# Performance work log

Hardware: AMD Instinct MI355X
Metric: run time of the kernel (lower is better)

## Reference

```python
import jax, jax.numpy as jnp
import numpy as np

D_MODEL = 1024
NUM_HEADS = 16
D_K = D_MODEL // NUM_HEADS
HEADS_DIST = [4, 4, 2, 2, 4]  # [token, statement, data_flow, control_flow, standard]
HYP_DF = 5.0
HYP_CF = 5.0
NEG_INF = -1000000000.0
B, S = 4, 1024


def _head_group_weights():
    # one-hot-per-group weight vectors of length NUM_HEADS
    ws = []
    start = 0
    for n in HEADS_DIST:
        w = np.zeros(NUM_HEADS, dtype=np.float32)
        w[start:start + n] = 1.0
        ws.append(jnp.asarray(w))
        start += n
    return ws  # tok_w, stmt_w, df_w, cf_w, std_w


def setup_inputs() -> dict:
    key = jax.random.key(0)
    ks = jax.random.split(key, 12)
    f32 = jnp.float32
    inp = {
        'Q': jax.random.normal(ks[0], (B, S, D_MODEL), f32),
        'K': jax.random.normal(ks[1], (B, S, D_MODEL), f32),
        'V': jax.random.normal(ks[2], (B, S, D_MODEL), f32),
        'token': jax.random.randint(ks[3], (B, S, S), 0, 2).astype(f32),
        'statement': jax.random.randint(ks[4], (B, S, S), 0, 2).astype(f32),
        'data_flow': jax.random.randint(ks[5], (B, S, S), 0, 2).astype(f32),
        'control_flow': jax.random.randint(ks[6], (B, S, S), 0, 2).astype(f32),
        'zero_matrix': jnp.zeros((B, S, S), f32),
        'mask': jax.random.randint(ks[7], (B, 1, S, S), 0, 2).astype(jnp.int32),
        # linear layer params (torch nn.Linear: y = x @ W.T + b)
        'Wq': jax.random.normal(ks[8], (D_MODEL, D_MODEL), f32) * 0.02,
        'bq': jnp.zeros((D_MODEL,), f32),
        'Wk': jax.random.normal(ks[9], (D_MODEL, D_MODEL), f32) * 0.02,
        'bk': jnp.zeros((D_MODEL,), f32),
        'Wv': jax.random.normal(ks[10], (D_MODEL, D_MODEL), f32) * 0.02,
        'bv': jnp.zeros((D_MODEL,), f32),
        'Wo': jax.random.normal(ks[11], (D_MODEL, D_MODEL), f32) * 0.02,
        'bo': jnp.zeros((D_MODEL,), f32),
    }
    return inp


def _split_heads(x):
    b, s, _ = x.shape
    return x.reshape(b, s, NUM_HEADS, D_K).transpose(0, 2, 1, 3)  # (B,H,S,dk)


def reference(Q, K, V, token, statement, data_flow, control_flow, zero_matrix,
              mask, Wq, bq, Wk, bk, Wv, bv, Wo, bo):
    tok_w, stmt_w, df_w, cf_w, _ = _head_group_weights()

    Qh = _split_heads(Q @ Wq.T + bq)
    Kh = _split_heads(K @ Wk.T + bk)
    Vh = _split_heads(V @ Wv.T + bv)

    scores = jnp.einsum('bhqd,bhkd->bhqk', Qh, Kh) / jnp.sqrt(jnp.float32(D_K))

    # local mask: -1e9 * token for token-heads, -1e9 * statement for statement-heads,
    # zero_matrix (zeros) elsewhere — expressed via per-head group weights instead of
    # the original redundant stack.
    w = lambda v: v[None, :, None, None]  # (1,H,1,1)
    local_mask = NEG_INF * (w(tok_w) * token[:, None] + w(stmt_w) * statement[:, None])
    # global enhance: |scores * (hyp_df*data_flow | hyp_cf*control_flow)| on their heads
    enhance_adj = (HYP_DF * w(df_w) * data_flow[:, None]
                   + HYP_CF * w(cf_w) * control_flow[:, None])
    global_enhance = jnp.abs(enhance_adj * scores)

    scores = scores + local_mask + global_enhance
    scores = jnp.where(mask == 0, NEG_INF, scores)

    probs = jax.nn.softmax(scores, axis=-1)  # (B,H,S,S)
    ctx = jnp.einsum('bhqk,bhkd->bhqd', probs, Vh)
    out = ctx.transpose(0, 2, 1, 3).reshape(B, S, D_MODEL)
    return out @ Wo.T + bo
```

## Files before the change

### kernel.cpp

```cpp
#include <hip/hip_runtime.h>
#include <stdint.h>

typedef unsigned short u16;
typedef unsigned int   u32;
typedef unsigned char  u8;
typedef __attribute__((ext_vector_type(4))) float f32x4;
typedef __attribute__((ext_vector_type(8))) __bf16 bf16x8;
typedef __attribute__((ext_vector_type(2))) unsigned int u32x2;
typedef __attribute__((ext_vector_type(4))) unsigned int u32x4;

#define MFMA16(a, b, c) __builtin_amdgcn_mfma_f32_16x16x32_bf16((a), (b), (c), 0, 0, 0)

__device__ __forceinline__ u16 f2bf(float f) {
  u32 u = __float_as_uint(f);
  return (u16)((u + 0x7fffu + ((u >> 16) & 1u)) >> 16);
}

__device__ __forceinline__ void gl_lds16(const void* g, void* l) {
  __builtin_amdgcn_global_load_lds((const __attribute__((address_space(1))) u32*)g,
                                   (__attribute__((address_space(3))) u32*)l, 16, 0, 0);
}

__device__ __forceinline__ u32 cvtpk(float a, float b) {
  u32 r;
  asm("v_cvt_pk_bf16_f32 %0, %1, %2" : "=v"(r) : "v"(a), "v"(b));
  return r;
}

__device__ __forceinline__ float exp2_hw(float x) {
  float r;
  asm("v_exp_f32 %0, %1" : "=v"(r) : "v"(x));
  return r;
}

__device__ __forceinline__ void plswap32(u32& x, u32& y) {
  u32x2 r = __builtin_amdgcn_permlane32_swap(x, y, false, false);
  x = r.x; y = r.y;
}
__device__ __forceinline__ void plswap16(u32& x, u32& y) {
  u32x2 r = __builtin_amdgcn_permlane16_swap(x, y, false, false);
  x = r.x; y = r.y;
}

__device__ __forceinline__ float redsum_lg(float v) {
  u32 x = __float_as_uint(v), y = x;
  plswap16(x, y);
  float m = __uint_as_float(x) + __uint_as_float(y);
  u32 a = __float_as_uint(m), b = a;
  plswap32(a, b);
  return __uint_as_float(a) + __uint_as_float(b);
}

__device__ __forceinline__ u32 pbit(float t, float s, float d, float c, int m) {
  const u32 nm = (m == 0) ? 1u : 0u;
  u32 r = (t != 0.0f ? 1u : 0u) | (s != 0.0f ? 2u : 0u) | (d != 0.0f ? 4u : 0u) |
          (c != 0.0f ? 8u : 0u) | ((1u - nm) << 4);
  r |= (((t != 0.0f ? 1u : 0u) | nm) << 5) | (((s != 0.0f ? 1u : 0u) | nm) << 6) | (nm << 7);
  return r;
}

__global__ void __launch_bounds__(256) pack_kernel(const float4* __restrict__ tok, const float4* __restrict__ st,
                                                   const float4* __restrict__ df, const float4* __restrict__ cf,
                                                   const int4* __restrict__ msk, u32* __restrict__ pko) {
  const int i = blockIdx.x * 256 + threadIdx.x;
  const int b = i >> 18, rem = i & 262143, q = rem >> 8, k4 = rem & 255;
  const int t = k4 >> 4, nk = (k4 >> 2) & 3, lg = k4 & 3;
  const u32 widx = ((u32)(b * 64 + (q >> 4)) * 16 + t) * 256 + (q & 15) * 16 + lg * 4 + nk;
  float4 vt = tok[i], vs = st[i], vd = df[i], vc = cf[i];
  int4 vm = msk[i];
  u32 b0 = pbit(vt.x, vs.x, vd.x, vc.x, vm.x);
  u32 b1 = pbit(vt.y, vs.y, vd.y, vc.y, vm.y);
  u32 b2 = pbit(vt.z, vs.z, vd.z, vc.z, vm.z);
  u32 b3 = pbit(vt.w, vs.w, vd.w, vc.w, vm.w);
  pko[widx] = b0 | (b1 << 8) | (b2 << 16) | (b3 << 24);
}

__global__ void __launch_bounds__(256) cvt_kernel(const float4* __restrict__ Q, const float4* __restrict__ K,
                                                  const float4* __restrict__ V, const float4* __restrict__ Wq,
                                                  const float4* __restrict__ Wk, const float4* __restrict__ Wv,
                                                  const float4* __restrict__ Wo, ushort4* __restrict__ oQ,
                                                  ushort4* __restrict__ oK, ushort4* __restrict__ oV,
                                                  ushort4* __restrict__ oWq, ushort4* __restrict__ oWk,
                                                  ushort4* __restrict__ oWv, ushort4* __restrict__ oWo) {
  const int bid = blockIdx.x;
  const float4* src;
  ushort4* dst;
  int base;
  if (bid < 1024)      { src = Q;  dst = oQ;  base = bid; }
  else if (bid < 2048) { src = K;  dst = oK;  base = bid - 1024; }
  else if (bid < 3072) { src = V;  dst = oV;  base = bid - 2048; }
  else if (bid < 3328) { src = Wq; dst = oWq; base = bid - 3072; }
  else if (bid < 3584) { src = Wk; dst = oWk; base = bid - 3328; }
  else if (bid < 3840) { src = Wv; dst = oWv; base = bid - 3584; }
  else                 { src = Wo; dst = oWo; base = bid - 3840; }
  const int i0 = base * 1024 + threadIdx.x;
#pragma unroll
  for (int u = 0; u < 4; u++) {
    const int i = i0 + u * 256;
    float4 v = src[i];
    dst[i] = make_ushort4(f2bf(v.x), f2bf(v.y), f2bf(v.z), f2bf(v.w));
  }
}

__global__ void __launch_bounds__(256) gemm_qkv(const u16* __restrict__ Abase, const u16* __restrict__ Wbase,
                                                const float* __restrict__ bq, const float* __restrict__ bk,
                                                const float* __restrict__ bv, u16* __restrict__ Obase) {
  __shared__ u16 smA[2][4096];
  __shared__ u16 smB[2][4096];
  const int fb = blockIdx.x;
  const int lid = (fb & 7) * 96 + (fb >> 3);
  const int z = lid >> 8;
  const int m0 = ((lid & 255) >> 3) * 128;
  const int n0 = (lid & 7) * 128;
  const u16* A = Abase + (size_t)z * 4194304;
  const u16* W = Wbase + (size_t)z * 1048576;
  const float* bias = (z == 0) ? bq : (z == 1) ? bk : bv;
  u16* Out = Obase + (size_t)z * 4194304;
  const int t = threadIdx.x;
  const int w = t >> 6, l = t & 63;
  const int l15 = l & 15, lg = l >> 4;
  const int wr = w >> 1, wc = w & 1;
  f32x4 acc[4][4] = {};
  const int srow = w * 16 + (l >> 2);
  const int scol_src = (((l & 3) ^ ((l >> 2) & 3))) * 8;
  const int scol_dst = (l & 3) * 8;
  const u16* Ab = A + (size_t)(m0 + srow) * 1024 + scol_src;
  const u16* Wb = W + (size_t)(n0 + srow) * 1024 + scol_src;
  const int soff = srow * 32 + scol_dst;
  const int c0g = (lg ^ (l15 & 3)) * 8;

  gl_lds16(Ab, &smA[0][soff]);
  gl_lds16(Ab + (size_t)64 * 1024, &smA[0][soff + 64 * 32]);
  gl_lds16(Wb, &smB[0][soff]);
  gl_lds16(Wb + (size_t)64 * 1024, &smB[0][soff + 64 * 32]);

  for (int it = 0; it < 32; it++) {
    __syncthreads();
    if (it < 31) {
      const int kk = (it + 1) * 32;
      const int nb = (it + 1) & 1;
      gl_lds16(Ab + kk, &smA[nb][soff]);
      gl_lds16(Ab + kk + (size_t)64 * 1024, &smA[nb][soff + 64 * 32]);
      gl_lds16(Wb + kk, &smB[nb][soff]);
      gl_lds16(Wb + kk + (size_t)64 * 1024, &smB[nb][soff + 64 * 32]);
    }
    const u16* bA = smA[it & 1];
    const u16* bB = smB[it & 1];
    bf16x8 af[4], bv_[4];
#pragma unroll
    for (int i = 0; i < 4; i++) af[i] = *(const bf16x8*)(bA + (wr * 64 + i * 16 + l15) * 32 + c0g);
#pragma unroll
    for (int i = 0; i < 4; i++) bv_[i] = *(const bf16x8*)(bB + (wc * 64 + i * 16 + l15) * 32 + c0g);
#pragma unroll
    for (int i = 0; i < 4; i++)
#pragma unroll
      for (int j = 0; j < 4; j++) acc[i][j] = MFMA16(af[i], bv_[j], acc[i][j]);
  }
#pragma unroll
  for (int j = 0; j < 4; j++) {
    const int n = n0 + wc * 64 + j * 16 + l15;
    const float bvj = bias[n];
#pragma unroll
    for (int i = 0; i < 4; i++) {
      const int mbase = m0 + wr * 64 + i * 16 + lg * 4;
      if (z < 2) {
#pragma unroll
        for (int r = 0; r < 4; r++) {
          const int m = mbase + r;
          Out[((size_t)((m >> 10) * 16 + (n >> 6)) << 16) + (size_t)(m & 1023) * 64 + (n & 63)] =
              f2bf(acc[i][j][r] + bvj);
        }
      } else {
        size_t off = ((size_t)((mbase >> 10) * 16 + (n >> 6)) << 16) + (size_t)(n & 63) * 1024 + (mbase & 1023);
        *(ushort4*)(Out + off) = make_ushort4(f2bf(acc[i][j][0] + bvj), f2bf(acc[i][j][1] + bvj),
                                              f2bf(acc[i][j][2] + bvj), f2bf(acc[i][j][3] + bvj));
      }
    }
  }
}

__global__ void __launch_bounds__(256) gemm_out(const u16* __restrict__ A, const u16* __restrict__ W,
                                                const float* __restrict__ bias, float* __restrict__ Out) {
  __shared__ u16 smA[2][4096];
  __shared__ u16 smB[2][4096];
  const int fb = blockIdx.x;
  const int lid = (fb & 7) * 32 + (fb >> 3);
  const int m0 = (lid >> 3) * 128;
  const int n0 = (lid & 7) * 128;
  const int t = threadIdx.x;
  const int w = t >> 6, l = t & 63;
  const int l15 = l & 15, lg = l >> 4;
  const int wr = w >> 1, wc = w & 1;
  f32x4 acc[4][4] = {};
  const int srow = w * 16 + (l >> 2);
  const int scol_src = (((l & 3) ^ ((l >> 2) & 3))) * 8;
  const int scol_dst = (l & 3) * 8;
  const u16* Ab = A + (size_t)(m0 + srow) * 1024 + scol_src;
  const u16* Wb = W + (size_t)(n0 + srow) * 1024 + scol_src;
  const int soff = srow * 32 + scol_dst;
  const int c0g = (lg ^ (l15 & 3)) * 8;

  gl_lds16(Ab, &smA[0][soff]);
  gl_lds16(Ab + (size_t)64 * 1024, &smA[0][soff + 64 * 32]);
  gl_lds16(Wb, &smB[0][soff]);
  gl_lds16(Wb + (size_t)64 * 1024, &smB[0][soff + 64 * 32]);

  for (int it = 0; it < 32; it++) {
    __syncthreads();
    if (it < 31) {
      const int kk = (it + 1) * 32;
      const int nb = (it + 1) & 1;
      gl_lds16(Ab + kk, &smA[nb][soff]);
      gl_lds16(Ab + kk + (size_t)64 * 1024, &smA[nb][soff + 64 * 32]);
      gl_lds16(Wb + kk, &smB[nb][soff]);
      gl_lds16(Wb + kk + (size_t)64 * 1024, &smB[nb][soff + 64 * 32]);
    }
    const u16* bA = smA[it & 1];
    const u16* bB = smB[it & 1];
    bf16x8 af[4], bv_[4];
#pragma unroll
    for (int i = 0; i < 4; i++) af[i] = *(const bf16x8*)(bA + (wr * 64 + i * 16 + l15) * 32 + c0g);
#pragma unroll
    for (int i = 0; i < 4; i++) bv_[i] = *(const bf16x8*)(bB + (wc * 64 + i * 16 + l15) * 32 + c0g);
#pragma unroll
    for (int i = 0; i < 4; i++)
#pragma unroll
      for (int j = 0; j < 4; j++) acc[i][j] = MFMA16(af[i], bv_[j], acc[i][j]);
  }
#pragma unroll
  for (int j = 0; j < 4; j++) {
    const int n = n0 + wc * 64 + j * 16 + l15;
    const float bvj = bias[n];
#pragma unroll
    for (int i = 0; i < 4; i++) {
      const int mbase = m0 + wr * 64 + i * 16 + lg * 4;
#pragma unroll
      for (int r = 0; r < 4; r++) Out[(size_t)(mbase + r) * 1024 + n] = acc[i][j][r] + bvj;
    }
  }
}

__global__ void __launch_bounds__(256) attn_kernel(const u16* __restrict__ Qp, const u16* __restrict__ Kp,
                                                   const u16* __restrict__ Vt, const u8* __restrict__ pack,
                                                   u16* __restrict__ ctx) {
  __shared__ u16 smK[2][4096];
  __shared__ u16 smV[2][4096];
  const float SCL  = 0.18033688011112042f;
  const float FMX  = 32.0f;
  const int tid = threadIdx.x;
  const int w = tid >> 6, l = tid & 63;
  const int l15 = l & 15, lg = l >> 4;
  const int f = blockIdx.x;
  const int swz = (f & 7) * 128 + (f >> 3);
  const int bh = swz >> 4, bx = swz & 15;
  const int b = bh >> 4, h = bh & 15;
  const int q0 = bx * 64 + w * 16;
  const bool enh = (h >= 8 && h < 12);
  const u32 kbit = (h < 4) ? 0x20u : (h < 8) ? 0x40u : 0x80u;
  const u32 ebit = (h < 10) ? 0x04u : 0x08u;
  const u32 kb_[4] = {kbit, kbit << 8, kbit << 16, kbit << 24};
  const u32 eb_[4] = {ebit, ebit << 8, ebit << 16, ebit << 24};
  const size_t hb = (size_t)bh << 16;

  bf16x8 qf[2];
#pragma unroll
  for (int ks = 0; ks < 2; ks++)
    qf[ks] = *(const bf16x8*)(Qp + hb + (size_t)(q0 + l15) * 64 + ks * 32 + lg * 8);

  const int srow = w * 16 + (l >> 3);
  const int schunk = (l & 7) ^ (l >> 3);
  const u16* Ksrc = Kp + hb + (size_t)srow * 64 + schunk * 8;
  const u16* Vsrc = Vt + hb + (size_t)srow * 1024 + schunk * 8;
  const int c0 = (lg ^ (l15 & 7)) * 8;
  const u8* pkq = pack + ((size_t)((b * 64 + bx * 4 + w) * 16)) * 1024 + (l15 * 4 + lg) * 16;

  gl_lds16(Ksrc, &smK[0][w * 1024]);
  gl_lds16(Ksrc + 512, &smK[0][w * 1024 + 512]);
  gl_lds16(Vsrc, &smV[0][w * 1024]);
  gl_lds16(Vsrc + 8192, &smV[0][w * 1024 + 512]);
  uint4 pk_next = *(const uint4*)(pkq);

  f32x4 octx[4] = {};
  float lrun = 0.0f;

  for (int t = 0; t < 16; t++) {
    __syncthreads();
    const uint4 pkc = pk_next;
    if (t < 15) {
      const int kb = (t + 1) * 64;
      const int nb = (t + 1) & 1;
      gl_lds16(Ksrc + (size_t)kb * 64, &smK[nb][w * 1024]);
      gl_lds16(Ksrc + (size_t)kb * 64 + 512, &smK[nb][w * 1024 + 512]);
      gl_lds16(Vsrc + kb, &smV[nb][w * 1024]);
      gl_lds16(Vsrc + kb + 8192, &smV[nb][w * 1024 + 512]);
      pk_next = *(const uint4*)(pkq + (t + 1) * 1024);
    }
    const u16* bK = smK[t & 1];
    const u16* bV = smV[t & 1];
    f32x4 sc[4];
#pragma unroll
    for (int nk = 0; nk < 4; nk++) {
      const u16* kr = bK + (nk * 16 + l15) * 64;
      bf16x8 kf0 = *(const bf16x8*)(kr + c0);
      bf16x8 kf1 = *(const bf16x8*)(kr + (c0 ^ 32));
      f32x4 z = {0.0f, 0.0f, 0.0f, 0.0f};
      z = MFMA16(kf0, qf[0], z);
      z = MFMA16(kf1, qf[1], z);
      sc[nk] = z;
    }
    const u32 pkw[4] = {pkc.x, pkc.y, pkc.z, pkc.w};
    float psum = 0.0f;
#pragma unroll
    for (int nk = 0; nk < 4; nk++)
#pragma unroll
      for (int r = 0; r < 4; r++) {
        float s;
        if (enh) {
          float tt = sc[nk][r] * SCL;
          tt = (pkw[nk] & eb_[r]) ? __builtin_fmaf(fabsf(tt), 5.0f, tt) : tt;
          s = tt - FMX;
        } else {
          s = __builtin_fmaf(sc[nk][r], SCL, -FMX);
        }
        float p = exp2_hw(s);
        p = (pkw[nk] & kb_[r]) ? 0.0f : p;
        sc[nk][r] = p;
        psum += p;
      }
    psum = redsum_lg(psum);
    lrun += psum;
#pragma unroll
    for (int kk = 0; kk < 2; kk++) {
      u32 a0 = cvtpk(sc[2 * kk][0], sc[2 * kk][1]);
      u32 a1 = cvtpk(sc[2 * kk][2], sc[2 * kk][3]);
      u32 b0 = cvtpk(sc[2 * kk + 1][0], sc[2 * kk + 1][1]);
      u32 b1 = cvtpk(sc[2 * kk + 1][2], sc[2 * kk + 1][3]);
      plswap32(a0, b0);
      plswap32(a1, b1);
      plswap16(a0, b0);
      plswap16(a1, b1);
      u32x4 wv = {a0, a1, b0, b1};
      bf16x8 pfrag = __builtin_bit_cast(bf16x8, wv);
#pragma unroll
      for (int nd = 0; nd < 4; nd++) {
        bf16x8 vf = *(const bf16x8*)(bV + (nd * 16 + l15) * 64 + (c0 ^ (kk * 32)));
        octx[nd] = MFMA16(vf, pfrag, octx[nd]);
      }
    }
  }
  const float inv = 1.0f / fmaxf(lrun, 1e-35f);
  u16* cb = ctx + (size_t)b * 1048576 + (size_t)(q0 + l15) * 1024 + h * 64 + lg * 4;
#pragma unroll
  for (int nd = 0; nd < 4; nd++) {
    *(ushort4*)(cb + nd * 16) = make_ushort4(f2bf(octx[nd][0] * inv), f2bf(octx[nd][1] * inv),
                                             f2bf(octx[nd][2] * inv), f2bf(octx[nd][3] * inv));
  }
}

extern "C" void kernel_launch(void* const* d_in, const int* in_sizes, int n_in,
                              void* d_out, int out_size, void* d_ws, size_t ws_size,
                              hipStream_t stream) {
  (void)in_sizes; (void)n_in; (void)out_size; (void)ws_size;
  const float* Q  = (const float*)d_in[0];
  const float* K  = (const float*)d_in[1];
  const float* V  = (const float*)d_in[2];
  const float* tok = (const float*)d_in[3];
  const float* st  = (const float*)d_in[4];
  const float* df  = (const float*)d_in[5];
  const float* cf  = (const float*)d_in[6];
  const int*   msk = (const int*)d_in[8];
  const float* Wq = (const float*)d_in[9];
  const float* bq = (const float*)d_in[10];
  const float* Wk = (const float*)d_in[11];
  const float* bk = (const float*)d_in[12];
  const float* Wv = (const float*)d_in[13];
  const float* bv = (const float*)d_in[14];
  const float* Wo = (const float*)d_in[15];
  const float* bo = (const float*)d_in[16];

  char* ws = (char*)d_ws;
  const size_t MB = 1ull << 20;
  u16* Qbf = (u16*)(ws);
  u16* Wqb = (u16*)(ws + 24 * MB);
  u8*  pkQ = (u8*)(ws + 32 * MB);
  u16* Qh  = (u16*)(ws + 36 * MB);
  u16* ctx = (u16*)(ws + 60 * MB);
  u16* Kbf = Qbf + 4194304;
  u16* Vbf = Qbf + 8388608;
  u16* Wkb = Wqb + 1048576;
  u16* Wvb = Wqb + 2097152;
  u16* Wob = Wqb + 3145728;

  pack_kernel<<<4096, 256, 0, stream>>>((const float4*)tok, (const float4*)st, (const float4*)df,
                                        (const float4*)cf, (const int4*)msk, (u32*)pkQ);
  cvt_kernel<<<4096, 256, 0, stream>>>((const float4*)Q, (const float4*)K, (const float4*)V,
                                       (const float4*)Wq, (const float4*)Wk, (const float4*)Wv, (const float4*)Wo,
                                       (ushort4*)Qbf, (ushort4*)Kbf, (ushort4*)Vbf,
                                       (ushort4*)Wqb, (ushort4*)Wkb, (ushort4*)Wvb, (ushort4*)Wob);
  gemm_qkv<<<768, 256, 0, stream>>>(Qbf, Wqb, bq, bk, bv, Qh);
  attn_kernel<<<1024, 256, 0, stream>>>(Qh, Qh + 4194304, Qh + 8388608, pkQ, ctx);
  gemm_out<<<256, 256, 0, stream>>>(ctx, Wob, bo, (float*)d_out);
}
```

Before: 135.8 us.

## Process 128 queries per attention block, two query tiles per wave

Each wave now handles 32 query rows (two 16-row MFMA tiles) instead of 16, so each K/V tile staged in LDS is reused across twice as many queries and the grid is halved to 512 blocks. The row-sum cross-lane reduction is deferred from every key tile to the end of the kernel. This cuts K/V global traffic and per-tile sync overhead per query, at the cost of more registers per thread and fewer blocks to spread across the CUs.

```diff
diff --git a/kernel.cpp b/kernel.cpp
--- a/kernel.cpp
+++ b/kernel.cpp
@@ -251,10 +251,10 @@
   const int w = tid >> 6, l = tid & 63;
   const int l15 = l & 15, lg = l >> 4;
   const int f = blockIdx.x;
-  const int swz = (f & 7) * 128 + (f >> 3);
-  const int bh = swz >> 4, bx = swz & 15;
+  const int swz = (f & 7) * 64 + (f >> 3);
+  const int bh = swz >> 3, bx = swz & 7;
   const int b = bh >> 4, h = bh & 15;
-  const int q0 = bx * 64 + w * 16;
+  const int q0 = bx * 128 + w * 32;
   const bool enh = (h >= 8 && h < 12);
   const u32 kbit = (h < 4) ? 0x20u : (h < 8) ? 0x40u : 0x80u;
   const u32 ebit = (h < 10) ? 0x04u : 0x08u;
@@ -262,30 +262,33 @@
   const u32 eb_[4] = {ebit, ebit << 8, ebit << 16, ebit << 24};
   const size_t hb = (size_t)bh << 16;
 
-  bf16x8 qf[2];
-#pragma unroll
-  for (int ks = 0; ks < 2; ks++)
-    qf[ks] = *(const bf16x8*)(Qp + hb + (size_t)(q0 + l15) * 64 + ks * 32 + lg * 8);
+  bf16x8 qf[2][2];
+#pragma unroll
+  for (int mq = 0; mq < 2; mq++)
+#pragma unroll
+    for (int ks = 0; ks < 2; ks++)
+      qf[mq][ks] = *(const bf16x8*)(Qp + hb + (size_t)(q0 + mq * 16 + l15) * 64 + ks * 32 + lg * 8);
 
   const int srow = w * 16 + (l >> 3);
   const int schunk = (l & 7) ^ (l >> 3);
   const u16* Ksrc = Kp + hb + (size_t)srow * 64 + schunk * 8;
   const u16* Vsrc = Vt + hb + (size_t)srow * 1024 + schunk * 8;
   const int c0 = (lg ^ (l15 & 7)) * 8;
-  const u8* pkq = pack + ((size_t)((b * 64 + bx * 4 + w) * 16)) * 1024 + (l15 * 4 + lg) * 16;
+  const u8* pkq0 = pack + ((size_t)((b * 64 + bx * 8 + w * 2) * 16)) * 1024 + (l15 * 4 + lg) * 16;
+  const u8* pkq1 = pkq0 + 16 * 1024;
 
   gl_lds16(Ksrc, &smK[0][w * 1024]);
   gl_lds16(Ksrc + 512, &smK[0][w * 1024 + 512]);
   gl_lds16(Vsrc, &smV[0][w * 1024]);
   gl_lds16(Vsrc + 8192, &smV[0][w * 1024 + 512]);
-  uint4 pk_next = *(const uint4*)(pkq);
-
-  f32x4 octx[4] = {};
-  float lrun = 0.0f;
+  uint4 pk_next[2] = {*(const uint4*)(pkq0), *(const uint4*)(pkq1)};
+
+  f32x4 octx[2][4] = {};
+  float lsum[2] = {0.0f, 0.0f};
 
   for (int t = 0; t < 16; t++) {
     __syncthreads();
-    const uint4 pkc = pk_next;
+    const uint4 pkc0 = pk_next[0], pkc1 = pk_next[1];
     if (t < 15) {
       const int kb = (t + 1) * 64;
       const int nb = (t + 1) & 1;
@@ -293,67 +296,82 @@
       gl_lds16(Ksrc + (size_t)kb * 64 + 512, &smK[nb][w * 1024 + 512]);
       gl_lds16(Vsrc + kb, &smV[nb][w * 1024]);
       gl_lds16(Vsrc + kb + 8192, &smV[nb][w * 1024 + 512]);
-      pk_next = *(const uint4*)(pkq + (t + 1) * 1024);
+      pk_next[0] = *(const uint4*)(pkq0 + (t + 1) * 1024);
+      pk_next[1] = *(const uint4*)(pkq1 + (t + 1) * 1024);
     }
     const u16* bK = smK[t & 1];
     const u16* bV = smV[t & 1];
-    f32x4 sc[4];
+    f32x4 sc[2][4];
 #pragma unroll
     for (int nk = 0; nk < 4; nk++) {
       const u16* kr = bK + (nk * 16 + l15) * 64;
       bf16x8 kf0 = *(const bf16x8*)(kr + c0);
       bf16x8 kf1 = *(const bf16x8*)(kr + (c0 ^ 32));
-      f32x4 z = {0.0f, 0.0f, 0.0f, 0.0f};
-      z = MFMA16(kf0, qf[0], z);
-      z = MFMA16(kf1, qf[1], z);
-      sc[nk] = z;
-    }
-    const u32 pkw[4] = {pkc.x, pkc.y, pkc.z, pkc.w};
-    float psum = 0.0f;
-#pragma unroll
-    for (int nk = 0; nk < 4; nk++)
-#pragma unroll
-      for (int r = 0; r < 4; r++) {
-        float s;
-        if (enh) {
-          float tt = sc[nk][r] * SCL;
-          tt = (pkw[nk] & eb_[r]) ? __builtin_fmaf(fabsf(tt), 5.0f, tt) : tt;
-          s = tt - FMX;
-        } else {
-          s = __builtin_fmaf(sc[nk][r], SCL, -FMX);
+#pragma unroll
+      for (int mq = 0; mq < 2; mq++) {
+        f32x4 z = {0.0f, 0.0f, 0.0f, 0.0f};
+        z = MFMA16(kf0, qf[mq][0], z);
+        z = MFMA16(kf1, qf[mq][1], z);
+        sc[mq][nk] = z;
+      }
+    }
+    const u32 pkw[2][4] = {{pkc0.x, pkc0.y, pkc0.z, pkc0.w}, {pkc1.x, pkc1.y, pkc1.z, pkc1.w}};
+#pragma unroll
+    for (int mq = 0; mq < 2; mq++) {
+      float ps = 0.0f;
+#pragma unroll
+      for (int nk = 0; nk < 4; nk++)
+#pragma unroll
+        for (int r = 0; r < 4; r++) {
+          float s;
+          if (enh) {
+            float tt = sc[mq][nk][r] * SCL;
+            tt = (pkw[mq][nk] & eb_[r]) ? __builtin_fmaf(fabsf(tt), 5.0f, tt) : tt;
+            s = tt - FMX;
+          } else {
+            s = __builtin_fmaf(sc[mq][nk][r], SCL, -FMX);
+          }
+          float p = exp2_hw(s);
+          p = (pkw[mq][nk] & kb_[r]) ? 0.0f : p;
+          sc[mq][nk][r] = p;
+          ps += p;
         }
-        float p = exp2_hw(s);
-        p = (pkw[nk] & kb_[r]) ? 0.0f : p;
-        sc[nk][r] = p;
-        psum += p;
+      lsum[mq] += ps;
+    }
+#pragma unroll
+    for (int kk = 0; kk < 2; kk++) {
+      bf16x8 pfrag[2];
+#pragma unroll
+      for (int mq = 0; mq < 2; mq++) {
+        u32 a0 = cvtpk(sc[mq][2 * kk][0], sc[mq][2 * kk][1]);
+        u32 a1 = cvtpk(sc[mq][2 * kk][2], sc[mq][2 * kk][3]);
+        u32 b0 = cvtpk(sc[mq][2 * kk + 1][0], sc[mq][2 * kk + 1][1]);
+        u32 b1 = cvtpk(sc[mq][2 * kk + 1][2], sc[mq][2 * kk + 1][3]);
+        plswap32(a0, b0);
+        plswap32(a1, b1);
+        plswap16(a0, b0);
+        plswap16(a1, b1);
+        u32x4 wv = {a0, a1, b0, b1};
+        pfrag[mq] = __builtin_bit_cast(bf16x8, wv);
       }
-    psum = redsum_lg(psum);
-    lrun += psum;
-#pragma unroll
-    for (int kk = 0; kk < 2; kk++) {
-      u32 a0 = cvtpk(sc[2 * kk][0], sc[2 * kk][1]);
-      u32 a1 = cvtpk(sc[2 * kk][2], sc[2 * kk][3]);
-      u32 b0 = cvtpk(sc[2 * kk + 1][0], sc[2 * kk + 1][1]);
-      u32 b1 = cvtpk(sc[2 * kk + 1][2], sc[2 * kk + 1][3]);
-      plswap32(a0, b0);
-      plswap32(a1, b1);
-      plswap16(a0, b0);
-      plswap16(a1, b1);
-      u32x4 wv = {a0, a1, b0, b1};
-      bf16x8 pfrag = __builtin_bit_cast(bf16x8, wv);
 #pragma unroll
       for (int nd = 0; nd < 4; nd++) {
         bf16x8 vf = *(const bf16x8*)(bV + (nd * 16 + l15) * 64 + (c0 ^ (kk * 32)));
-        octx[nd] = MFMA16(vf, pfrag, octx[nd]);
+        octx[0][nd] = MFMA16(vf, pfrag[0], octx[0][nd]);
+        octx[1][nd] = MFMA16(vf, pfrag[1], octx[1][nd]);
       }
     }
   }
-  const float inv = 1.0f / fmaxf(lrun, 1e-35f);
-  u16* cb = ctx + (size_t)b * 1048576 + (size_t)(q0 + l15) * 1024 + h * 64 + lg * 4;
-#pragma unroll
-  for (int nd = 0; nd < 4; nd++) {
-    *(ushort4*)(cb + nd * 16) = make_ushort4(f2bf(octx[nd][0] * inv), f2bf(octx[nd][1] * inv),
-                                             f2bf(octx[nd][2] * inv), f2bf(octx[nd][3] * inv));
+#pragma unroll
+  for (int mq = 0; mq < 2; mq++) {
+    const float lr = redsum_lg(lsum[mq]);
+    const float inv = 1.0f / fmaxf(lr, 1e-35f);
+    u16* cb = ctx + (size_t)b * 1048576 + (size_t)(q0 + mq * 16 + l15) * 1024 + h * 64 + lg * 4;
+#pragma unroll
+    for (int nd = 0; nd < 4; nd++) {
+      *(ushort4*)(cb + nd * 16) = make_ushort4(f2bf(octx[mq][nd][0] * inv), f2bf(octx[mq][nd][1] * inv),
+                                               f2bf(octx[mq][nd][2] * inv), f2bf(octx[mq][nd][3] * inv));
+    }
   }
 }
 
@@ -398,6 +416,6 @@
                                        (ushort4*)Qbf, (ushort4*)Kbf, (ushort4*)Vbf,
                                        (ushort4*)Wqb, (ushort4*)Wkb, (ushort4*)Wvb, (ushort4*)Wob);
   gemm_qkv<<<768, 256, 0, stream>>>(Qbf, Wqb, bq, bk, bv, Qh);
-  attn_kernel<<<1024, 256, 0, stream>>>(Qh, Qh + 4194304, Qh + 8388608, pkQ, ctx);
+  attn_kernel<<<512, 256, 0, stream>>>(Qh, Qh + 4194304, Qh + 8388608, pkQ, ctx);
   gemm_out<<<256, 256, 0, stream>>>(ctx, Wob, bo, (float*)d_out);
 }
```

Result: slower. 141.6 us (+4.2%).
